# Performance work log

Hardware: AMD Instinct MI355X
Metric: run time of the kernel (lower is better)

Reference implementation:

```python
import jax, jax.numpy as jnp
import numpy as np

HIDDEN_DIM = 2048
HEAD_NUM = 16
HEAD_DIM = HIDDEN_DIM // HEAD_NUM


def setup_inputs() -> dict:
    key = jax.random.key(0)
    ks = jax.random.split(key, 9)
    B, S, H = 2, 2048, HIDDEN_DIM
    scale = 1.0 / np.sqrt(H)
    X = jax.random.normal(ks[0], (B, S, H), dtype=jnp.float32)
    Wq = jax.random.normal(ks[1], (H, H), dtype=jnp.float32) * scale
    bq = jnp.zeros((H,), dtype=jnp.float32)
    Wk = jax.random.normal(ks[2], (H, H), dtype=jnp.float32) * scale
    bk = jnp.zeros((H,), dtype=jnp.float32)
    Wv = jax.random.normal(ks[3], (H, H), dtype=jnp.float32) * scale
    bv = jnp.zeros((H,), dtype=jnp.float32)
    Wo = jax.random.normal(ks[4], (H, H), dtype=jnp.float32) * scale
    bo = jnp.zeros((H,), dtype=jnp.float32)
    return {"X": X, "Wq": Wq, "bq": bq, "Wk": Wk, "bk": bk,
            "Wv": Wv, "bv": bv, "Wo": Wo, "bo": bo}


def reference(X, Wq, bq, Wk, bk, Wv, bv, Wo, bo):
    B, S, H = X.shape
    # QKV projections (nn.Linear applies x @ W.T + b; weights here stored as [in, out])
    Q = X @ Wq + bq
    K = X @ Wk + bk
    V = X @ Wv + bv
    # [B, heads, S, head_dim]
    q = Q.reshape(B, S, HEAD_NUM, HEAD_DIM).transpose(0, 2, 1, 3)
    k = K.reshape(B, S, HEAD_NUM, HEAD_DIM).transpose(0, 2, 1, 3)
    v = V.reshape(B, S, HEAD_NUM, HEAD_DIM).transpose(0, 2, 1, 3)
    scores = jnp.einsum('bhqd,bhkd->bhqk', q, k) / jnp.sqrt(jnp.float32(HEAD_DIM))
    attn = jax.nn.softmax(scores, axis=-1)  # dropout = identity in eval
    out = jnp.einsum('bhqk,bhkd->bhqd', attn, v)
    out = out.transpose(0, 2, 1, 3).reshape(B, S, H)
    return out @ Wo + bo
```

## Files before the change

### kernel.cpp

```cpp
#include <hip/hip_runtime.h>
#include <hip/hip_bf16.h>
#include <stdint.h>


#define Bc 2
#define Sc 2048
#define Hc 2048
#define NHc 16
#define Dc 128
#define Mc 4096

typedef unsigned short ushortT;
typedef float f32x4 __attribute__((ext_vector_type(4)));
typedef _Float16 f16x8 __attribute__((ext_vector_type(8)));

#define MFMAH(a, b, c) __builtin_amdgcn_mfma_f32_16x16x32_f16((a), (b), (c), 0, 0, 0)

static __device__ __forceinline__ ushortT f2h(float x) {
    _Float16 h = (_Float16)x;
    return __builtin_bit_cast(unsigned short, h);
}

static __device__ __forceinline__ void load_lds16(const ushortT* g, ushortT* l) {
    __builtin_amdgcn_global_load_lds(
        (__attribute__((address_space(1))) void*)(g),
        (__attribute__((address_space(3))) void*)(l), 16, 0, 0);
}

__global__ __launch_bounds__(256) void pack_a(
    const float* __restrict__ src, ushortT* __restrict__ dst)
{
    const int mt = blockIdx.x, kt = blockIdx.y;
    const int t = threadIdx.x;
    const int kq = t & 15;
    const int r0 = t >> 4;
    ushortT* tile = dst + ((size_t)(mt * 32 + kt)) * 8192;
#pragma unroll
    for (int rr = 0; rr < 8; ++rr) {
        const int row = r0 + rr * 16;
        const float4 v = *(const float4*)(src + (size_t)(mt * 128 + row) * Hc + kt * 64 + kq * 4);
        _Float16 h[4] = {(_Float16)v.x, (_Float16)v.y, (_Float16)v.z, (_Float16)v.w};
        const int gid = kq >> 1, halfg = kq & 1;
        const int gp = gid ^ (row & 7);
        *(uint2*)(tile + (size_t)row * 64 + gp * 8 + halfg * 4) = *(uint2*)h;
    }
}

__global__ __launch_bounds__(256) void pack_b(
    const float* __restrict__ W0, const float* __restrict__ W1,
    const float* __restrict__ W2, const float* __restrict__ W3,
    ushortT* __restrict__ dst)
{
    const int nt = blockIdx.x, kt = blockIdx.y, which = blockIdx.z;
    const float* W = (which == 0) ? W0 : (which == 1) ? W1 : (which == 2) ? W2 : W3;
    const int t = threadIdx.x;
    const int n = t & 127;
    const int g0 = (t >> 7) * 4;
    ushortT* tile = dst + (size_t)which * 4194304 + ((size_t)(nt * 32 + kt)) * 8192;
#pragma unroll
    for (int gi = 0; gi < 4; ++gi) {
        const int g = g0 + gi;
        _Float16 h[8];
#pragma unroll
        for (int j = 0; j < 8; ++j)
            h[j] = (_Float16)W[(size_t)(kt * 64 + g * 8 + j) * Hc + nt * 128 + n];
        const int gp = g ^ (n & 7);
        *(uint4*)(tile + (size_t)n * 64 + gp * 8) = *(uint4*)h;
    }
}

#define GEMM_PROLOGUE()                                                        \
    __shared__ __align__(16) ushortT As[8192], Bs[8192];                       \
    const int tid = threadIdx.x, wv_ = tid >> 6, lane = tid & 63;              \
    const int lane16 = lane & 15, quad = lane >> 4;                            \
    const int quad4 = quad * 4;                                                \
    const int wm = (wv_ & 1) * 64, wn = (wv_ >> 1) * 64;                       \
    int aoff[4][2], boff[4][2];                                                \
    _Pragma("unroll") for (int mi = 0; mi < 4; ++mi)                           \
        _Pragma("unroll") for (int kf = 0; kf < 2; ++kf) {                     \
            const int ra = wm + mi * 16 + lane16;                              \
            aoff[mi][kf] = ra * 64 + (((kf * 4 + quad) ^ (ra & 7)) << 3);      \
            const int rb = wn + mi * 16 + lane16;                              \
            boff[mi][kf] = rb * 64 + (((kf * 4 + quad) ^ (rb & 7)) << 3);      \
        }                                                                      \
    f32x4 acc[4][4];                                                           \
    _Pragma("unroll") for (int i = 0; i < 4; ++i)                              \
        _Pragma("unroll") for (int j = 0; j < 4; ++j) {                        \
            acc[i][j][0] = 0.f; acc[i][j][1] = 0.f;                            \
            acc[i][j][2] = 0.f; acc[i][j][3] = 0.f; }                          \
    ushortT* asd = &As[wv_ * 2048];                                            \
    ushortT* bsd = &Bs[wv_ * 2048];

#define GEMM_KLOOP(at, bt)                                                     \
    for (int kt2 = 0; kt2 < 32; ++kt2) {                                       \
        _Pragma("unroll") for (int i = 0; i < 4; ++i) {                        \
            load_lds16(at + i * 512 + lane * 8, asd + i * 512);                \
            load_lds16(bt + i * 512 + lane * 8, bsd + i * 512);                \
        }                                                                      \
        at += 8192; bt += 8192;                                                \
        __syncthreads();                                                       \
        _Pragma("unroll") for (int kf = 0; kf < 2; ++kf) {                     \
            f16x8 a[4], b[4];                                                  \
            _Pragma("unroll") for (int mi = 0; mi < 4; ++mi)                   \
                a[mi] = *(const f16x8*)&As[aoff[mi][kf]];                      \
            _Pragma("unroll") for (int nj = 0; nj < 4; ++nj)                   \
                b[nj] = *(const f16x8*)&Bs[boff[nj][kf]];                      \
            _Pragma("unroll") for (int nj = 0; nj < 4; ++nj)                   \
                _Pragma("unroll") for (int mi = 0; mi < 4; ++mi)               \
                    acc[mi][nj] = MFMAH(a[mi], b[nj], acc[mi][nj]);            \
        }                                                                      \
        __syncthreads();                                                       \
    }

#define G256_PROLOGUE()                                                        \
    __shared__ __align__(16) ushortT LA[2][2][8192];                           \
    __shared__ __align__(16) ushortT LB[2][2][8192];                           \
    const int tid = threadIdx.x, wv_ = tid >> 6, lane = tid & 63;              \
    const int lane16 = lane & 15, quad = lane >> 4, quad4 = (lane >> 4) * 4;   \
    const int wr = wv_ >> 2, wc = wv_ & 3;                                     \
    const ushortT* LAr = &LA[0][0][0] + wr * 8192;                             \
    const ushortT* LBr = &LB[0][0][0] + (wc >> 1) * 8192;                      \
    int oA[2][4][2], oB[4][2];                                                 \
    _Pragma("unroll") for (int h = 0; h < 2; ++h)                              \
        _Pragma("unroll") for (int mi = 0; mi < 4; ++mi)                       \
            _Pragma("unroll") for (int kf = 0; kf < 2; ++kf) {                 \
                const int r_ = h * 64 + mi * 16 + lane16;                      \
                oA[h][mi][kf] = r_ * 64 + (((kf * 4 + quad) ^ (r_ & 7)) << 3); \
            }                                                                  \
    _Pragma("unroll") for (int nj = 0; nj < 4; ++nj)                           \
        _Pragma("unroll") for (int kf = 0; kf < 2; ++kf) {                     \
            const int r_ = (wc & 1) * 64 + nj * 16 + lane16;                   \
            oB[nj][kf] = r_ * 64 + (((kf * 4 + quad) ^ (r_ & 7)) << 3);        \
        }                                                                      \
    f32x4 acc[8][4];                                                           \
    _Pragma("unroll") for (int i = 0; i < 8; ++i)                              \
        _Pragma("unroll") for (int j = 0; j < 4; ++j) {                        \
            acc[i][j][0] = 0.f; acc[i][j][1] = 0.f;                            \
            acc[i][j][2] = 0.f; acc[i][j][3] = 0.f; }

#define STAGE(SRC, STEP, DST) do {                                             \
    const ushortT* g_ = (SRC) + (size_t)(STEP) * 8192;                         \
    ushortT* l_ = (DST) + wv_ * 1024;                                          \
    load_lds16(g_, l_);                                                        \
    load_lds16(g_ + 512, l_ + 512);                                            \
} while (0)

#define RD_A(S, H)                                                             \
    _Pragma("unroll") for (int mi = 0; mi < 4; ++mi)                           \
        _Pragma("unroll") for (int kf = 0; kf < 2; ++kf)                       \
            a[mi][kf] = *(const f16x8*)&LAr[(S) * 16384 + oA[H][mi][kf]];

#define RD_B(S)                                                                \
    _Pragma("unroll") for (int nj = 0; nj < 4; ++nj)                           \
        _Pragma("unroll") for (int kf = 0; kf < 2; ++kf)                       \
            b[nj][kf] = *(const f16x8*)&LBr[(S) * 16384 + oB[nj][kf]];

#define QUAD(MIB, NJB)                                                         \
    _Pragma("unroll") for (int kf = 0; kf < 2; ++kf)                           \
        _Pragma("unroll") for (int mi = 0; mi < 4; ++mi)                       \
            _Pragma("unroll") for (int nj = 0; nj < 2; ++nj)                   \
                acc[(MIB) + mi][(NJB) + nj] =                                  \
                    MFMAH(a[mi][kf], b[(NJB) + nj][kf], acc[(MIB) + mi][(NJB) + nj]);

#define PRE_MFMA()                                                             \
    __builtin_amdgcn_s_barrier();                                              \
    __builtin_amdgcn_s_setprio(1);

#define POST_MFMA()                                                            \
    __builtin_amdgcn_s_setprio(0);                                             \
    __builtin_amdgcn_s_barrier();

#define VMC6() asm volatile("s_waitcnt vmcnt(6)" ::: "memory")

#define MINS(x) ((x) < 31 ? (x) : 31)

#define G256_MAIN(AB0, AB1, BB0, BB1)                                          \
    const ushortT* sA0 = (AB0) + wv_ * 1024 + lane * 8;                        \
    const ushortT* sA1 = (AB1) + wv_ * 1024 + lane * 8;                        \
    const ushortT* sB0 = (BB0) + wv_ * 1024 + lane * 8;                        \
    const ushortT* sB1 = (BB1) + wv_ * 1024 + lane * 8;                        \
      \
    STAGE(sB0, 0, &LB[0][0][0]); STAGE(sB1, 0, &LB[0][1][0]);                  \
    STAGE(sA0, 0, &LA[0][0][0]); STAGE(sA1, 0, &LA[0][1][0]);                  \
    STAGE(sB0, 1, &LB[1][0][0]); STAGE(sB1, 1, &LB[1][1][0]);                  \
    STAGE(sA0, 1, &LA[1][0][0]);                                               \
    VMC6();                                                                    \
    __builtin_amdgcn_s_barrier();                                              \
    _Pragma("clang loop unroll(disable)")                                      \
    for (int t = 0; t < 32; t += 2) {                                          \
        f16x8 a[4][2], b[4][2];                                                \
                                \
        RD_A(0, 0); RD_B(0);                                                   \
        STAGE(sA1, t + 1, &LA[1][1][0]);                                       \
        PRE_MFMA(); QUAD(0, 0); POST_MFMA();                                   \
                                            \
        STAGE(sB0, MINS(t + 2), &LB[0][0][0]);                                 \
        PRE_MFMA(); QUAD(0, 2); POST_MFMA();                                   \
                                                       \
        RD_A(0, 1);                                                            \
        STAGE(sB1, MINS(t + 2), &LB[0][1][0]);                                 \
        PRE_MFMA(); QUAD(4, 2); POST_MFMA();                                   \
            \
        STAGE(sA0, MINS(t + 2), &LA[0][0][0]);                                 \
        VMC6();                                                                \
        PRE_MFMA(); QUAD(4, 0); POST_MFMA();                                   \
                                             \
        RD_A(1, 0); RD_B(1);                                                   \
        STAGE(sA1, MINS(t + 2), &LA[0][1][0]);                                 \
        PRE_MFMA(); QUAD(0, 0); POST_MFMA();                                   \
                                                                       \
        STAGE(sB0, MINS(t + 3), &LB[1][0][0]);                                 \
        PRE_MFMA(); QUAD(0, 2); POST_MFMA();                                   \
                                                                       \
        RD_A(1, 1);                                                            \
        STAGE(sB1, MINS(t + 3), &LB[1][1][0]);                                 \
        PRE_MFMA(); QUAD(4, 2); POST_MFMA();                                   \
                            \
        STAGE(sA0, MINS(t + 3), &LA[1][0][0]);                                 \
        VMC6();                                                                \
        PRE_MFMA(); QUAD(4, 0); POST_MFMA();                                   \
    }

__global__ __launch_bounds__(512, 2) void qkv_gemm256(
    const ushortT* __restrict__ Xp, const ushortT* __restrict__ Wall,
    const float* __restrict__ bq, const float* __restrict__ bk,
    const float* __restrict__ bv,
    ushortT* __restrict__ Qd, ushortT* __restrict__ Kd, ushortT* __restrict__ Vt)
{
    const int id = blockIdx.x;
    const int swz = (id & 7) * 48 + (id >> 3);
    const int mt = swz & 15;
    const int bn = swz >> 4;
    const int which = bn >> 3, bnw = bn & 7;
    const ushortT* Ab0 = Xp + (size_t)((2 * mt + 0) * 32) * 8192;
    const ushortT* Ab1 = Xp + (size_t)((2 * mt + 1) * 32) * 8192;
    const ushortT* Wp  = Wall + (size_t)which * 4194304;
    const ushortT* Bb0 = Wp + (size_t)((bnw * 2 + 0) * 32) * 8192;
    const ushortT* Bb1 = Wp + (size_t)((bnw * 2 + 1) * 32) * 8192;
    const float* bias = (which == 0) ? bq : (which == 1) ? bk : bv;

    G256_PROLOGUE();
    G256_MAIN(Ab0, Ab1, Bb0, Bb1);
    asm volatile("s_waitcnt vmcnt(0)" ::: "memory");

    const float QS = 0.08838834764831845f * 1.4426950408889634f;
#pragma unroll
    for (int nj = 0; nj < 4; ++nj) {
        const int colm = bnw * 256 + wc * 64 + nj * 16 + lane16;
        const float bb2 = bias[colm];
        const int hh = colm >> 7, dd = colm & 127;
#pragma unroll
        for (int mi = 0; mi < 8; ++mi) {
            const int m0 = mt * 256 + wr * 128 + mi * 16 + quad4;
            const int b = m0 >> 11, s0_ = m0 & 2047;
            const size_t bhb = (size_t)(b * NHc + hh) * (Sc * Dc);
            if (which == 0) {
#pragma unroll
                for (int r = 0; r < 4; ++r) {
                    const float v = acc[mi][nj][r] + bb2;
                    Qd[bhb + (size_t)(s0_ + r) * Dc + dd] = f2h(v * QS);
                }
            } else if (which == 1) {
#pragma unroll
                for (int r = 0; r < 4; ++r) {
                    const float v = acc[mi][nj][r] + bb2;
                    const int s = s0_ + r;
                    const int t2 = s >> 6, sin_ = s & 63;
                    Kd[bhb + (size_t)t2 * 8192 + sin_ * 128 +
                       (((dd >> 3) ^ (sin_ & 7)) << 3) + (dd & 7)] = f2h(v);
                }
            } else {
                const int t2 = s0_ >> 6, sin0 = s0_ & 63;
                uint2 u;
                u.x = (uint32_t)f2h(acc[mi][nj][0] + bb2) |
                      ((uint32_t)f2h(acc[mi][nj][1] + bb2) << 16);
                u.y = (uint32_t)f2h(acc[mi][nj][2] + bb2) |
                      ((uint32_t)f2h(acc[mi][nj][3] + bb2) << 16);
                *(uint2*)&Vt[bhb + (size_t)t2 * 8192 + dd * 64 +
                             (((sin0 >> 3) ^ (dd & 7)) << 3) + (sin0 & 7)] = u;
            }
        }
    }
}

__global__ __launch_bounds__(128, 2) void attn(
    const ushortT* __restrict__ Qd, const ushortT* __restrict__ Kt,
    const ushortT* __restrict__ Vt, ushortT* __restrict__ AOp)
{
    const int id = blockIdx.x;
    const int slot = id >> 3;
    const int pair = (id & 7) + ((slot >> 5) << 3);
    const int qt = slot & 31;
    const int hh = pair & 15, bb = pair >> 4;

    const ushortT* Qp  = Qd + ((size_t)(bb * NHc + hh)) * Sc * Dc;
    const ushortT* Kbh = Kt + ((size_t)(bb * NHc + hh)) * Sc * Dc;
    const ushortT* Vbh = Vt + ((size_t)(bb * NHc + hh)) * Sc * Dc;

    __shared__ __align__(16) ushortT Ks[8192];
    __shared__ __align__(16) ushortT Vs[8192];
    __shared__ __align__(16) ushortT Pbuf[2][2048];

    const int tid = threadIdx.x, wv_ = tid >> 6, lane = tid & 63;
    const int lane16 = lane & 15, quad = lane >> 4;
    const int quad8 = quad * 8, quad4 = quad * 4;
    const int s0 = qt * 64 + wv_ * 32;

    f16x8 q[2][4];
#pragma unroll
    for (int nj = 0; nj < 2; ++nj)
#pragma unroll
        for (int kf = 0; kf < 4; ++kf)
            q[nj][kf] = *(const f16x8*)(Qp + (size_t)(s0 + nj * 16 + lane16) * Dc + kf * 32 + quad8);

    f32x4 o[8][2];
#pragma unroll
    for (int dj = 0; dj < 8; ++dj)
#pragma unroll
        for (int nj = 0; nj < 2; ++nj) { o[dj][nj][0] = 0.f; o[dj][nj][1] = 0.f; o[dj][nj][2] = 0.f; o[dj][nj][3] = 0.f; }

    float m_run[2] = {-1e30f, -1e30f}, l_run[2] = {0.f, 0.f};
    ushortT* Pw = Pbuf[wv_];

    for (int nt = 0; nt < 32; ++nt) {
        const ushortT* ktile = Kbh + (size_t)nt * 8192 + wv_ * 4096;
        const ushortT* vtile = Vbh + (size_t)nt * 8192 + wv_ * 4096;
#pragma unroll
        for (int i = 0; i < 8; ++i) {
            load_lds16(ktile + i * 512 + lane * 8, Ks + wv_ * 4096 + i * 512);
            load_lds16(vtile + i * 512 + lane * 8, Vs + wv_ * 4096 + i * 512);
        }
        __syncthreads();

        f32x4 sacc[4][2];
#pragma unroll
        for (int mi = 0; mi < 4; ++mi)
#pragma unroll
            for (int nj = 0; nj < 2; ++nj) { sacc[mi][nj][0] = 0.f; sacc[mi][nj][1] = 0.f; sacc[mi][nj][2] = 0.f; sacc[mi][nj][3] = 0.f; }
#pragma unroll
        for (int kf = 0; kf < 4; ++kf) {
            f16x8 kb[4];
#pragma unroll
            for (int mi = 0; mi < 4; ++mi) {
                const int row = mi * 16 + lane16;
                kb[mi] = *(const f16x8*)&Ks[row * 128 + (((kf * 4 + quad) ^ (row & 7)) << 3)];
            }
#pragma unroll
            for (int mi = 0; mi < 4; ++mi)
#pragma unroll
                for (int nj = 0; nj < 2; ++nj)
                    sacc[mi][nj] = MFMAH(kb[mi], q[nj][kf], sacc[mi][nj]);
        }

        float alpha_[2];
#pragma unroll
        for (int nj = 0; nj < 2; ++nj) {
            float mx = sacc[0][nj][0];
#pragma unroll
            for (int mi = 0; mi < 4; ++mi)
#pragma unroll
                for (int r = 0; r < 4; ++r) mx = fmaxf(mx, sacc[mi][nj][r]);
            mx = fmaxf(mx, __shfl_xor(mx, 16));
            mx = fmaxf(mx, __shfl_xor(mx, 32));
            const float mnew = fmaxf(m_run[nj], mx);
            alpha_[nj] = exp2f(m_run[nj] - mnew);
            m_run[nj] = mnew;
            float sum = 0.f;
#pragma unroll
            for (int mi = 0; mi < 4; ++mi)
#pragma unroll
                for (int r = 0; r < 4; ++r) {
                    const float p = exp2f(sacc[mi][nj][r] - mnew);
                    sacc[mi][nj][r] = p;
                    sum += p;
                }
            sum += __shfl_xor(sum, 16);
            sum += __shfl_xor(sum, 32);
            l_run[nj] = l_run[nj] * alpha_[nj] + sum;
            const int prow = nj * 16 + lane16;
#pragma unroll
            for (int mi = 0; mi < 4; ++mi) {
                uint2 u;
                u.x = (uint32_t)f2h(sacc[mi][nj][0]) | ((uint32_t)f2h(sacc[mi][nj][1]) << 16);
                u.y = (uint32_t)f2h(sacc[mi][nj][2]) | ((uint32_t)f2h(sacc[mi][nj][3]) << 16);
                const int g = mi * 2 + (quad >> 1);
                *(uint2*)&Pw[prow * 64 + ((g ^ (prow & 7)) << 3) + (quad & 1) * 4] = u;
            }
        }

#pragma unroll
        for (int dj = 0; dj < 8; ++dj)
#pragma unroll
            for (int nj = 0; nj < 2; ++nj) {
                const float av = alpha_[nj];
                o[dj][nj][0] *= av; o[dj][nj][1] *= av;
                o[dj][nj][2] *= av; o[dj][nj][3] *= av;
            }

#pragma unroll
        for (int kf2 = 0; kf2 < 2; ++kf2) {
            f16x8 pb[2];
#pragma unroll
            for (int nj = 0; nj < 2; ++nj) {
                const int row = nj * 16 + lane16;
                pb[nj] = *(const f16x8*)&Pw[row * 64 + (((kf2 * 4 + quad) ^ (row & 7)) << 3)];
            }
#pragma unroll
            for (int dj = 0; dj < 8; ++dj) {
                const int row = dj * 16 + lane16;
                const f16x8 vb = *(const f16x8*)&Vs[row * 64 + (((kf2 * 4 + quad) ^ (row & 7)) << 3)];
#pragma unroll
                for (int nj = 0; nj < 2; ++nj)
                    o[dj][nj] = MFMAH(vb, pb[nj], o[dj][nj]);
            }
        }
        __syncthreads();
    }

#pragma unroll
    for (int nj = 0; nj < 2; ++nj) {
        const float inv = 1.f / l_run[nj];
        const int m = bb * Sc + qt * 64 + wv_ * 32 + nj * 16 + lane16;
        const int mtile = m >> 7, rin = m & 127;
#pragma unroll
        for (int dj = 0; dj < 8; ++dj) {
            const int ktile = hh * 2 + (dj >> 2);
            const int cin0 = (dj & 3) * 16 + quad4;
            const int g = cin0 >> 3, e0 = cin0 & 7;
            uint2 u;
            u.x = (uint32_t)f2h(o[dj][nj][0] * inv) | ((uint32_t)f2h(o[dj][nj][1] * inv) << 16);
            u.y = (uint32_t)f2h(o[dj][nj][2] * inv) | ((uint32_t)f2h(o[dj][nj][3] * inv) << 16);
            *(uint2*)&AOp[((size_t)(mtile * 32 + ktile)) * 8192 + rin * 64 +
                          ((g ^ (rin & 7)) << 3) + e0] = u;
        }
    }
}

__global__ __launch_bounds__(256) void out_gemm(
    const ushortT* __restrict__ AOp, const ushortT* __restrict__ Wop,
    const float* __restrict__ bo, float* __restrict__ out)
{
    const int nt = blockIdx.x;
    const int mt = blockIdx.y;

    GEMM_PROLOGUE();

    const ushortT* at = AOp + (size_t)(mt * 32) * 8192 + wv_ * 2048;
    const ushortT* bt = Wop + (size_t)(nt * 32) * 8192 + wv_ * 2048;
    GEMM_KLOOP(at, bt);

#pragma unroll
    for (int nj = 0; nj < 4; ++nj) {
        const int col = nt * 128 + wn + nj * 16 + lane16;
        const float bb = bo[col];
#pragma unroll
        for (int mi = 0; mi < 4; ++mi)
#pragma unroll
            for (int r = 0; r < 4; ++r) {
                const int m = mt * 128 + wm + mi * 16 + quad4 + r;
                out[(size_t)m * Hc + col] = acc[mi][nj][r] + bb;
            }
    }
}

extern "C" void kernel_launch(void* const* d_in, const int* in_sizes, int n_in,
                              void* d_out, int out_size, void* d_ws, size_t ws_size,
                              hipStream_t stream) {
    (void)in_sizes; (void)n_in; (void)out_size; (void)ws_size;

    const float* X  = (const float*)d_in[0];
    const float* Wq = (const float*)d_in[1];
    const float* bq = (const float*)d_in[2];
    const float* Wk = (const float*)d_in[3];
    const float* bk = (const float*)d_in[4];
    const float* Wv = (const float*)d_in[5];
    const float* bv = (const float*)d_in[6];
    const float* Wo = (const float*)d_in[7];
    const float* bo = (const float*)d_in[8];
    float* out = (float*)d_out;

    ushortT* ws = (ushortT*)d_ws;
    const size_t E = (size_t)Mc * Hc;
    const size_t WE = (size_t)Hc * Hc;
    ushortT* Xp   = ws;
    ushortT* Wall = Xp + E;
    ushortT* Qd   = Wall + 4 * WE;
    ushortT* Kd   = Qd + E;
    ushortT* Vtp  = Kd + E;
    ushortT* AOp  = Vtp + E;

    pack_a<<<dim3(32, 32), 256, 0, stream>>>(X, Xp);
    pack_b<<<dim3(16, 32, 4), 256, 0, stream>>>(Wq, Wk, Wv, Wo, Wall);
    qkv_gemm256<<<dim3(384), 512, 0, stream>>>(Xp, Wall, bq, bk, bv, Qd, Kd, Vtp);
    attn<<<dim3(1024), 128, 0, stream>>>(Qd, Kd, Vtp, AOp);
    out_gemm<<<dim3(16, 32), 256, 0, stream>>>(AOp, Wall + 3 * WE, bo, out);
}
```

Measured before the change: 446.1 us.

## Transpose MFMA operands for Q/K projection epilogue, skip unit rescale, raise MFMA priority

For the Q and K outputs of the QKV GEMM, the MFMA operand order is swapped so each lane holds four consecutive columns. This lets the epilogue load bias as a float4 and write packed 8-byte stores instead of scalar 2-byte stores. The V path keeps the original order. In attention, the output accumulator rescale is skipped when every lane's alpha is 1, and s_setprio wraps the MFMA loops. Duplicating the GEMM main loop in two branches increases code size and could raise register pressure.

Result: no change. 450.8 us (+1.1%).

```diff
diff --git a/kernel.cpp b/kernel.cpp
--- a/kernel.cpp
+++ b/kernel.cpp
@@ -15,6 +15,8 @@
 typedef _Float16 f16x8 __attribute__((ext_vector_type(8)));
 
 #define MFMAH(a, b, c) __builtin_amdgcn_mfma_f32_16x16x32_f16((a), (b), (c), 0, 0, 0)
+#define MF_AB(a, b, c) MFMAH((a), (b), (c))
+#define MF_BA(a, b, c) MFMAH((b), (a), (c))
 
 static __device__ __forceinline__ ushortT f2h(float x) {
     _Float16 h = (_Float16)x;
@@ -155,12 +157,12 @@
         _Pragma("unroll") for (int kf = 0; kf < 2; ++kf)                       \
             b[nj][kf] = *(const f16x8*)&LBr[(S) * 16384 + oB[nj][kf]];
 
-#define QUAD(MIB, NJB)                                                         \
+#define QUAD(MIB, NJB, MF)                                                     \
     _Pragma("unroll") for (int kf = 0; kf < 2; ++kf)                           \
         _Pragma("unroll") for (int mi = 0; mi < 4; ++mi)                       \
             _Pragma("unroll") for (int nj = 0; nj < 2; ++nj)                   \
                 acc[(MIB) + mi][(NJB) + nj] =                                  \
-                    MFMAH(a[mi][kf], b[(NJB) + nj][kf], acc[(MIB) + mi][(NJB) + nj]);
+                    MF(a[mi][kf], b[(NJB) + nj][kf], acc[(MIB) + mi][(NJB) + nj]);
 
 #define PRE_MFMA()                                                             \
     __builtin_amdgcn_s_barrier();                                              \
@@ -174,7 +176,7 @@
 
 #define MINS(x) ((x) < 31 ? (x) : 31)
 
-#define G256_MAIN(AB0, AB1, BB0, BB1)                                          \
+#define G256_MAIN(AB0, AB1, BB0, BB1, MF)                                      \
     const ushortT* sA0 = (AB0) + wv_ * 1024 + lane * 8;                        \
     const ushortT* sA1 = (AB1) + wv_ * 1024 + lane * 8;                        \
     const ushortT* sB0 = (BB0) + wv_ * 1024 + lane * 8;                        \
@@ -192,33 +194,33 @@
                                 \
         RD_A(0, 0); RD_B(0);                                                   \
         STAGE(sA1, t + 1, &LA[1][1][0]);                                       \
-        PRE_MFMA(); QUAD(0, 0); POST_MFMA();                                   \
+        PRE_MFMA(); QUAD(0, 0, MF); POST_MFMA();                               \
                                             \
         STAGE(sB0, MINS(t + 2), &LB[0][0][0]);                                 \
-        PRE_MFMA(); QUAD(0, 2); POST_MFMA();                                   \
+        PRE_MFMA(); QUAD(0, 2, MF); POST_MFMA();                               \
                                                        \
         RD_A(0, 1);                                                            \
         STAGE(sB1, MINS(t + 2), &LB[0][1][0]);                                 \
-        PRE_MFMA(); QUAD(4, 2); POST_MFMA();                                   \
+        PRE_MFMA(); QUAD(4, 2, MF); POST_MFMA();                               \
             \
         STAGE(sA0, MINS(t + 2), &LA[0][0][0]);                                 \
         VMC6();                                                                \
-        PRE_MFMA(); QUAD(4, 0); POST_MFMA();                                   \
+        PRE_MFMA(); QUAD(4, 0, MF); POST_MFMA();                               \
                                              \
         RD_A(1, 0); RD_B(1);                                                   \
         STAGE(sA1, MINS(t + 2), &LA[0][1][0]);                                 \
-        PRE_MFMA(); QUAD(0, 0); POST_MFMA();                                   \
+        PRE_MFMA(); QUAD(0, 0, MF); POST_MFMA();                               \
                                                                        \
         STAGE(sB0, MINS(t + 3), &LB[1][0][0]);                                 \
-        PRE_MFMA(); QUAD(0, 2); POST_MFMA();                                   \
+        PRE_MFMA(); QUAD(0, 2, MF); POST_MFMA();                               \
                                                                        \
         RD_A(1, 1);                                                            \
         STAGE(sB1, MINS(t + 3), &LB[1][1][0]);                                 \
-        PRE_MFMA(); QUAD(4, 2); POST_MFMA();                                   \
+        PRE_MFMA(); QUAD(4, 2, MF); POST_MFMA();                               \
                             \
         STAGE(sA0, MINS(t + 3), &LA[1][0][0]);                                 \
         VMC6();                                                                \
-        PRE_MFMA(); QUAD(4, 0); POST_MFMA();                                   \
+        PRE_MFMA(); QUAD(4, 0, MF); POST_MFMA();                               \
     }
 
 __global__ __launch_bounds__(512, 2) void qkv_gemm256(
@@ -240,36 +242,23 @@
     const float* bias = (which == 0) ? bq : (which == 1) ? bk : bv;
 
     G256_PROLOGUE();
-    G256_MAIN(Ab0, Ab1, Bb0, Bb1);
-    asm volatile("s_waitcnt vmcnt(0)" ::: "memory");
 
     const float QS = 0.08838834764831845f * 1.4426950408889634f;
-#pragma unroll
-    for (int nj = 0; nj < 4; ++nj) {
-        const int colm = bnw * 256 + wc * 64 + nj * 16 + lane16;
-        const float bb2 = bias[colm];
-        const int hh = colm >> 7, dd = colm & 127;
-#pragma unroll
-        for (int mi = 0; mi < 8; ++mi) {
-            const int m0 = mt * 256 + wr * 128 + mi * 16 + quad4;
-            const int b = m0 >> 11, s0_ = m0 & 2047;
-            const size_t bhb = (size_t)(b * NHc + hh) * (Sc * Dc);
-            if (which == 0) {
-#pragma unroll
-                for (int r = 0; r < 4; ++r) {
-                    const float v = acc[mi][nj][r] + bb2;
-                    Qd[bhb + (size_t)(s0_ + r) * Dc + dd] = f2h(v * QS);
-                }
-            } else if (which == 1) {
-#pragma unroll
-                for (int r = 0; r < 4; ++r) {
-                    const float v = acc[mi][nj][r] + bb2;
-                    const int s = s0_ + r;
-                    const int t2 = s >> 6, sin_ = s & 63;
-                    Kd[bhb + (size_t)t2 * 8192 + sin_ * 128 +
-                       (((dd >> 3) ^ (sin_ & 7)) << 3) + (dd & 7)] = f2h(v);
-                }
-            } else {
+
+    if (which == 2) {
+        G256_MAIN(Ab0, Ab1, Bb0, Bb1, MF_AB);
+        asm volatile("s_waitcnt vmcnt(0)" ::: "memory");
+#pragma unroll
+        for (int nj = 0; nj < 4; ++nj) {
+            const int colm = bnw * 256 + wc * 64 + nj * 16 + lane16;
+            const float bb2 = bias[colm];
+            const int dd = colm & 127;
+            const int hh = colm >> 7;
+#pragma unroll
+            for (int mi = 0; mi < 8; ++mi) {
+                const int m0 = mt * 256 + wr * 128 + mi * 16 + quad4;
+                const int b = m0 >> 11, s0_ = m0 & 2047;
+                const size_t bhb = (size_t)(b * NHc + hh) * (Sc * Dc);
                 const int t2 = s0_ >> 6, sin0 = s0_ & 63;
                 uint2 u;
                 u.x = (uint32_t)f2h(acc[mi][nj][0] + bb2) |
@@ -278,6 +267,39 @@
                       ((uint32_t)f2h(acc[mi][nj][3] + bb2) << 16);
                 *(uint2*)&Vt[bhb + (size_t)t2 * 8192 + dd * 64 +
                              (((sin0 >> 3) ^ (dd & 7)) << 3) + (sin0 & 7)] = u;
+            }
+        }
+    } else {
+        G256_MAIN(Ab0, Ab1, Bb0, Bb1, MF_BA);
+        asm volatile("s_waitcnt vmcnt(0)" ::: "memory");
+#pragma unroll
+        for (int nj = 0; nj < 4; ++nj) {
+            const int col0 = bnw * 256 + wc * 64 + nj * 16 + quad4;
+            const float4 bv4 = *(const float4*)&bias[col0];
+            const int dd0 = col0 & 127;
+            const int hh = col0 >> 7;
+#pragma unroll
+            for (int mi = 0; mi < 8; ++mi) {
+                const int m = mt * 256 + wr * 128 + mi * 16 + lane16;
+                const int b = m >> 11, s = m & 2047;
+                const size_t bhb = (size_t)(b * NHc + hh) * (Sc * Dc);
+                float v0 = acc[mi][nj][0] + bv4.x;
+                float v1 = acc[mi][nj][1] + bv4.y;
+                float v2 = acc[mi][nj][2] + bv4.z;
+                float v3 = acc[mi][nj][3] + bv4.w;
+                if (which == 0) {
+                    uint2 u;
+                    u.x = (uint32_t)f2h(v0 * QS) | ((uint32_t)f2h(v1 * QS) << 16);
+                    u.y = (uint32_t)f2h(v2 * QS) | ((uint32_t)f2h(v3 * QS) << 16);
+                    *(uint2*)&Qd[bhb + (size_t)s * Dc + dd0] = u;
+                } else {
+                    const int t2 = s >> 6, sin_ = s & 63;
+                    uint2 u;
+                    u.x = (uint32_t)f2h(v0) | ((uint32_t)f2h(v1) << 16);
+                    u.y = (uint32_t)f2h(v2) | ((uint32_t)f2h(v3) << 16);
+                    *(uint2*)&Kd[bhb + (size_t)t2 * 8192 + sin_ * 128 +
+                                 (((dd0 >> 3) ^ (sin_ & 7)) << 3) + (dd0 & 7)] = u;
+                }
             }
         }
     }
@@ -337,6 +359,7 @@
         for (int mi = 0; mi < 4; ++mi)
 #pragma unroll
             for (int nj = 0; nj < 2; ++nj) { sacc[mi][nj][0] = 0.f; sacc[mi][nj][1] = 0.f; sacc[mi][nj][2] = 0.f; sacc[mi][nj][3] = 0.f; }
+        __builtin_amdgcn_s_setprio(1);
 #pragma unroll
         for (int kf = 0; kf < 4; ++kf) {
             f16x8 kb[4];
@@ -351,6 +374,7 @@
                 for (int nj = 0; nj < 2; ++nj)
                     sacc[mi][nj] = MFMAH(kb[mi], q[nj][kf], sacc[mi][nj]);
         }
+        __builtin_amdgcn_s_setprio(0);
 
         float alpha_[2];
 #pragma unroll
@@ -388,15 +412,18 @@
             }
         }
 
-#pragma unroll
-        for (int dj = 0; dj < 8; ++dj)
-#pragma unroll
-            for (int nj = 0; nj < 2; ++nj) {
-                const float av = alpha_[nj];
-                o[dj][nj][0] *= av; o[dj][nj][1] *= av;
-                o[dj][nj][2] *= av; o[dj][nj][3] *= av;
-            }
-
+        if (__ballot((alpha_[0] != 1.f) | (alpha_[1] != 1.f)) != 0ull) {
+#pragma unroll
+            for (int dj = 0; dj < 8; ++dj)
+#pragma unroll
+                for (int nj = 0; nj < 2; ++nj) {
+                    const float av = alpha_[nj];
+                    o[dj][nj][0] *= av; o[dj][nj][1] *= av;
+                    o[dj][nj][2] *= av; o[dj][nj][3] *= av;
+                }
+        }
+
+        __builtin_amdgcn_s_setprio(1);
 #pragma unroll
         for (int kf2 = 0; kf2 < 2; ++kf2) {
             f16x8 pb[2];
@@ -414,6 +441,7 @@
                     o[dj][nj] = MFMAH(vb, pb[nj], o[dj][nj]);
             }
         }
+        __builtin_amdgcn_s_setprio(0);
         __syncthreads();
     }
 
```
